# Kernel optimization log

Hardware: AMD Instinct MI355X
Metric: run time of the kernel (lower is better)

Reference implementation:

```python
import jax, jax.numpy as jnp
import numpy as np

DIM = 64
NUM_HEADS = 2
HEAD_DIM = DIM // NUM_HEADS


def setup_inputs() -> dict:
    key = jax.random.key(0)
    k1, k2, k3 = jax.random.split(key, 3)
    b, c, h, w = 8, DIM, 256, 256
    x = jax.random.normal(k1, (b, c, h, w), dtype=jnp.float32)
    # 1x1 conv weights, stored as [out_ch, in_ch] (kernel spatial dims are 1)
    qkv_w = jax.random.normal(k2, (3 * c, c), dtype=jnp.float32) * (1.0 / np.sqrt(c))
    proj_w = jax.random.normal(k3, (c, c), dtype=jnp.float32) * (1.0 / np.sqrt(c))
    return {"x": x, "qkv_w": qkv_w, "proj_w": proj_w}


def _phi(t):
    # elu(x) + 1 feature map (positive-valued kernel features)
    return jax.nn.elu(t) + 1.0


def reference(x, qkv_w, proj_w):
    b, c, h, w = x.shape
    n = h * w
    # 1x1 conv == per-pixel channel matmul
    qkv = jnp.einsum('oc,bchw->bohw', qkv_w, x)  # [b, 3c, h, w]
    q, k, v = jnp.split(qkv, 3, axis=1)

    def reshape(t):
        return t.reshape(b, NUM_HEADS, HEAD_DIM, n)  # bhcn

    q_phi = _phi(reshape(q))
    k_phi = _phi(reshape(k))
    v_h = reshape(v)
    # KV outer product over the sequence dim: tiny [b, h, c, d]
    KV = jnp.einsum('bhcn,bhdn->bhcd', k_phi, v_h)
    out_h = jnp.einsum('bhcn,bhcd->bhdn', q_phi, KV)  # [b, h, d, n]
    out = out_h.reshape(b, c, h, w)
    return jnp.einsum('oc,bchw->bohw', proj_w, out)
```

## Files before the change

### kernel.cpp

```cpp
#include <hip/hip_runtime.h>
#include <hip/hip_bf16.h>

#define BATCH 8
#define CH    64
#define NPIX  65536
#define NHEAD 2
#define HDIM  32
#define P1_BLOCKS 128

typedef __attribute__((ext_vector_type(8))) short bf16x8;
typedef __attribute__((ext_vector_type(4))) float f32x4;

#define MFMA(a, b, c) __builtin_amdgcn_mfma_f32_16x16x32_bf16(a, b, c, 0, 0, 0)

__device__ __forceinline__ unsigned rne_pk(float lo, float hi) {
    unsigned ua = __float_as_uint(lo); ua += 0x7fffu + ((ua >> 16) & 1u);
    unsigned ub = __float_as_uint(hi); ub += 0x7fffu + ((ub >> 16) & 1u);
    return (ua >> 16) | (ub & 0xffff0000u);
}

__device__ __forceinline__ bf16x8 pack8(const float* f) {
    int4 iv;
    iv.x = (int)rne_pk(f[0], f[1]);
    iv.y = (int)rne_pk(f[2], f[3]);
    iv.z = (int)rne_pk(f[4], f[5]);
    iv.w = (int)rne_pk(f[6], f[7]);
    return *reinterpret_cast<bf16x8*>(&iv);
}

__device__ __forceinline__ float phi_f(float t) {
    return t > 0.0f ? t + 1.0f : __expf(t);
}

__device__ __forceinline__ bf16x8 load_w_frag(const float* W, int r0, int k0, int lane) {
    const float* p = W + (size_t)(r0 + (lane & 15)) * 64 + k0 + ((lane >> 4) << 3);
    float f[8];
    #pragma unroll
    for (int e = 0; e < 8; e++) f[e] = p[e];
    return pack8(f);
}

__global__ __launch_bounds__(256) void la_pass1(
    const float* __restrict__ x, const float* __restrict__ qkv_w,
    float* __restrict__ partials, unsigned short* __restrict__ xt)
{
    __shared__ __align__(16) unsigned char smem[40960];

    const int tid  = threadIdx.x;
    const int lane = tid & 63;
    const int wv   = __builtin_amdgcn_readfirstlane(tid >> 6);
    const int b    = blockIdx.y;
    const int g    = lane >> 4;
    const int li   = lane & 15;

    unsigned short* kls = (unsigned short*)(smem + wv * 10240);
    unsigned short* vls = kls + 64 * 40;

    bf16x8 Wf[8][2];
    #pragma unroll
    for (int j = 0; j < 8; j++)
        #pragma unroll
        for (int ks = 0; ks < 2; ks++)
            Wf[j][ks] = load_w_frag(qkv_w, 64 + 16 * j, 32 * ks, lane);

    f32x4 kvacc[2][2][2];
    #pragma unroll
    for (int h = 0; h < 2; h++)
        #pragma unroll
        for (int mt = 0; mt < 2; mt++)
            #pragma unroll
            for (int nt = 0; nt < 2; nt++)
                kvacc[h][mt][nt] = (f32x4){0.f, 0.f, 0.f, 0.f};

    const float* xb = x + (size_t)b * CH * NPIX;
    unsigned short* xtb = xt + (size_t)b * NPIX * CH;

    for (int s = blockIdx.x * 4 + wv; s < 2048; s += P1_BLOCKS * 4) {
        const int px0 = s * 32;

        bf16x8 xa[2][2];
        #pragma unroll
        for (int mt = 0; mt < 2; mt++) {
            const float* xp = xb + px0 + 16 * mt + li;
            #pragma unroll
            for (int ks = 0; ks < 2; ks++) {
                float f[8];
                #pragma unroll
                for (int e = 0; e < 8; e++)
                    f[e] = xp[(size_t)(32 * ks + 8 * g + e) * NPIX];
                xa[mt][ks] = pack8(f);
            }
        }

        #pragma unroll
        for (int mt = 0; mt < 2; mt++)
            #pragma unroll
            for (int ks = 0; ks < 2; ks++)
                *reinterpret_cast<int4*>(xtb + (size_t)(px0 + 16 * mt + li) * CH + 32 * ks + 8 * g) =
                    *reinterpret_cast<const int4*>(&xa[mt][ks]);

        #pragma unroll
        for (int j = 0; j < 8; j++) {
            unsigned short* dst = (j < 4) ? kls : vls;
            const int crow = (j & 3) * 16 + li;
            #pragma unroll
            for (int mt = 0; mt < 2; mt++) {
                f32x4 acc = (f32x4){0.f, 0.f, 0.f, 0.f};
                acc = MFMA(xa[mt][0], Wf[j][0], acc);
                acc = MFMA(xa[mt][1], Wf[j][1], acc);
                float v0 = acc[0], v1 = acc[1], v2 = acc[2], v3 = acc[3];
                if (j < 4) { v0 = phi_f(v0); v1 = phi_f(v1); v2 = phi_f(v2); v3 = phi_f(v3); }
                *reinterpret_cast<uint2*>(dst + crow * 40 + 16 * mt + 4 * g) =
                    make_uint2(rne_pk(v0, v1), rne_pk(v2, v3));
            }
        }

        #pragma unroll
        for (int h = 0; h < 2; h++) {
            bf16x8 af[2], bv[2];
            #pragma unroll
            for (int mt = 0; mt < 2; mt++)
                af[mt] = *reinterpret_cast<const bf16x8*>(kls + (32 * h + 16 * mt + li) * 40 + 8 * g);
            #pragma unroll
            for (int nt = 0; nt < 2; nt++)
                bv[nt] = *reinterpret_cast<const bf16x8*>(vls + (32 * h + 16 * nt + li) * 40 + 8 * g);
            #pragma unroll
            for (int mt = 0; mt < 2; mt++)
                #pragma unroll
                for (int nt = 0; nt < 2; nt++)
                    kvacc[h][mt][nt] = MFMA(af[mt], bv[nt], kvacc[h][mt][nt]);
        }
    }

    __syncthreads();
    float* rbuf = (float*)smem;
    #pragma unroll
    for (int h = 0; h < 2; h++)
        #pragma unroll
        for (int mt = 0; mt < 2; mt++)
            #pragma unroll
            for (int nt = 0; nt < 2; nt++) {
                const int t = (h * 2 + mt) * 2 + nt;
                #pragma unroll
                for (int r = 0; r < 4; r++)
                    rbuf[wv * 2048 + t * 256 + (4 * g + r) * 16 + li] = kvacc[h][mt][nt][r];
            }
    __syncthreads();

    float* outp = partials + ((size_t)b * P1_BLOCKS + blockIdx.x) * 2048;
    #pragma unroll
    for (int i = 0; i < 8; i++) {
        const int idx = i * 256 + tid;
        const float sum = rbuf[idx] + rbuf[2048 + idx] + rbuf[4096 + idx] + rbuf[6144 + idx];
        const int t = idx >> 8, within = idx & 255;
        const int row = within >> 4, col = within & 15;
        const int h = t >> 2, mt = (t >> 1) & 1, nt = t & 1;
        outp[(h * 32 + 16 * mt + row) * 32 + 16 * nt + col] = sum;
    }
}

__global__ __launch_bounds__(256) void la_reduce(
    const float* __restrict__ partials, float* __restrict__ kv)
{
    const int b = blockIdx.x >> 3;
    const int e = (blockIdx.x & 7) * 256 + threadIdx.x;
    const float* p = partials + (size_t)b * P1_BLOCKS * 2048 + e;
    float s0 = 0.f, s1 = 0.f, s2 = 0.f, s3 = 0.f;
    #pragma unroll 8
    for (int j = 0; j < P1_BLOCKS; j += 4) {
        s0 += p[(size_t)j * 2048];
        s1 += p[(size_t)(j + 1) * 2048];
        s2 += p[(size_t)(j + 2) * 2048];
        s3 += p[(size_t)(j + 3) * 2048];
    }
    kv[(size_t)b * 2048 + e] = (s0 + s1) + (s2 + s3);
}

__global__ __launch_bounds__(256) void la_pass2(
    const unsigned short* __restrict__ xt, const float* __restrict__ qkv_w,
    const float* __restrict__ proj_w, const float* __restrict__ kv,
    float* __restrict__ y)
{
    __shared__ __align__(16) unsigned short sm2[4][2][16][72];

    const int tid  = threadIdx.x;
    const int lane = tid & 63;
    const int wv   = __builtin_amdgcn_readfirstlane(tid >> 6);
    const int b    = blockIdx.y;
    const int g    = lane >> 4;
    const int li   = lane & 15;

    unsigned short* qT = &sm2[wv][0][0][0];
    unsigned short* oT = &sm2[wv][1][0][0];

    bf16x8 Aq[4][2], Ap[4][2], Akv[2][2];
    #pragma unroll
    for (int mt = 0; mt < 4; mt++)
        #pragma unroll
        for (int ks = 0; ks < 2; ks++) {
            Aq[mt][ks] = load_w_frag(qkv_w, 16 * mt, 32 * ks, lane);
            Ap[mt][ks] = load_w_frag(proj_w, 16 * mt, 32 * ks, lane);
        }
    const float* kvb = kv + (size_t)b * NHEAD * HDIM * HDIM;
    #pragma unroll
    for (int h = 0; h < 2; h++)
        #pragma unroll
        for (int mtd = 0; mtd < 2; mtd++) {
            float f[8];
            #pragma unroll
            for (int e = 0; e < 8; e++)
                f[e] = kvb[h * 1024 + (8 * g + e) * 32 + 16 * mtd + li];
            Akv[h][mtd] = pack8(f);
        }

    const unsigned short* xtb = xt + (size_t)b * NPIX * CH;
    float*                yb  = y  + (size_t)b * CH * NPIX;

    for (int s = blockIdx.x * 4 + wv; s < 4096; s += 1024) {
        const int px0 = s * 16;

        bf16x8 bx[2];
        const unsigned short* xp = xtb + (size_t)(px0 + li) * CH + 8 * g;
        #pragma unroll
        for (int ks = 0; ks < 2; ks++)
            bx[ks] = *reinterpret_cast<const bf16x8*>(xp + 32 * ks);

        #pragma unroll
        for (int mt = 0; mt < 4; mt++) {
            f32x4 acc = (f32x4){0.f, 0.f, 0.f, 0.f};
            acc = MFMA(Aq[mt][0], bx[0], acc);
            acc = MFMA(Aq[mt][1], bx[1], acc);
            const float p0 = phi_f(acc[0]), p1 = phi_f(acc[1]);
            const float p2 = phi_f(acc[2]), p3 = phi_f(acc[3]);
            *reinterpret_cast<uint2*>(qT + li * 72 + 16 * mt + 4 * g) =
                make_uint2(rne_pk(p0, p1), rne_pk(p2, p3));
        }

        #pragma unroll
        for (int h = 0; h < 2; h++) {
            const bf16x8 bq = *reinterpret_cast<const bf16x8*>(qT + li * 72 + 32 * h + 8 * g);
            #pragma unroll
            for (int mtd = 0; mtd < 2; mtd++) {
                f32x4 acc = (f32x4){0.f, 0.f, 0.f, 0.f};
                acc = MFMA(Akv[h][mtd], bq, acc);
                *reinterpret_cast<uint2*>(oT + li * 72 + 32 * h + 16 * mtd + 4 * g) =
                    make_uint2(rne_pk(acc[0], acc[1]), rne_pk(acc[2], acc[3]));
            }
        }

        const bf16x8 bo0 = *reinterpret_cast<const bf16x8*>(oT + li * 72 + 8 * g);
        const bf16x8 bo1 = *reinterpret_cast<const bf16x8*>(oT + li * 72 + 32 + 8 * g);
        #pragma unroll
        for (int mt = 0; mt < 4; mt++) {
            f32x4 acc = (f32x4){0.f, 0.f, 0.f, 0.f};
            acc = MFMA(Ap[mt][0], bo0, acc);
            acc = MFMA(Ap[mt][1], bo1, acc);
            #pragma unroll
            for (int r = 0; r < 4; r++)
                yb[(size_t)(16 * mt + 4 * g + r) * NPIX + px0 + li] = acc[r];
        }
    }
}

extern "C" void kernel_launch(void* const* d_in, const int* in_sizes, int n_in,
                              void* d_out, int out_size, void* d_ws, size_t ws_size,
                              hipStream_t stream) {
    (void)in_sizes; (void)n_in; (void)out_size; (void)ws_size;
    const float* x      = (const float*)d_in[0];
    const float* qkv_w  = (const float*)d_in[1];
    const float* proj_w = (const float*)d_in[2];
    float* yout = (float*)d_out;

    unsigned short* xt      = (unsigned short*)d_ws;
    float*          partials = (float*)(xt + (size_t)BATCH * NPIX * CH);
    float*          kv       = partials + (size_t)BATCH * P1_BLOCKS * 2048;

    la_pass1 <<<dim3(P1_BLOCKS, BATCH), dim3(256), 0, stream>>>(x, qkv_w, partials, xt);
    la_reduce<<<dim3(64),               dim3(256), 0, stream>>>(partials, kv);
    la_pass2 <<<dim3(256, BATCH),       dim3(256), 0, stream>>>(xt, qkv_w, proj_w, kv, yout);
}
```

Before: 132.2 us.

## Stage x tiles through LDS with coalesced float4 loads in pass1

Pass1 now loads a 64x128 pixel tile of x cooperatively, with each lane reading float4 along the pixel dimension. It converts the tile to bf16 in shared memory, and the waves then gather MFMA fragments from LDS instead of issuing strided scalar global loads per channel. The k/v LDS row pitch is changed from 40 to 36 elements, with fragment reads split into two 8-byte loads. This adds block-wide barriers around each tile and uses more shared memory, which may reduce occupancy.

```diff
diff --git a/kernel.cpp b/kernel.cpp
--- a/kernel.cpp
+++ b/kernel.cpp
@@ -32,6 +32,13 @@
     return t > 0.0f ? t + 1.0f : __expf(t);
 }
 
+__device__ __forceinline__ bf16x8 lds_read8(const unsigned short* p) {
+    uint2 a = *reinterpret_cast<const uint2*>(p);
+    uint2 b = *reinterpret_cast<const uint2*>(p + 4);
+    int4 iv; iv.x = (int)a.x; iv.y = (int)a.y; iv.z = (int)b.x; iv.w = (int)b.y;
+    return *reinterpret_cast<bf16x8*>(&iv);
+}
+
 __device__ __forceinline__ bf16x8 load_w_frag(const float* W, int r0, int k0, int lane) {
     const float* p = W + (size_t)(r0 + (lane & 15)) * 64 + k0 + ((lane >> 4) << 3);
     float f[8];
@@ -44,7 +51,8 @@
     const float* __restrict__ x, const float* __restrict__ qkv_w,
     float* __restrict__ partials, unsigned short* __restrict__ xt)
 {
-    __shared__ __align__(16) unsigned char smem[40960];
+    __shared__ __align__(16) unsigned char smem[53248];
+    unsigned short* xls = (unsigned short*)smem;
 
     const int tid  = threadIdx.x;
     const int lane = tid & 63;
@@ -52,9 +60,11 @@
     const int b    = blockIdx.y;
     const int g    = lane >> 4;
     const int li   = lane & 15;
-
-    unsigned short* kls = (unsigned short*)(smem + wv * 10240);
-    unsigned short* vls = kls + 64 * 40;
+    const int l32  = lane & 31;
+    const int lhi  = lane >> 5;
+
+    unsigned short* kls = (unsigned short*)(smem + 16384 + wv * 9216);
+    unsigned short* vls = kls + 64 * 36;
 
     bf16x8 Wf[8][2];
     #pragma unroll
@@ -75,29 +85,47 @@
     const float* xb = x + (size_t)b * CH * NPIX;
     unsigned short* xtb = xt + (size_t)b * NPIX * CH;
 
-    for (int s = blockIdx.x * 4 + wv; s < 2048; s += P1_BLOCKS * 4) {
-        const int px0 = s * 32;
+    for (int it = 0; it < 4; it++) {
+        const int px0 = (blockIdx.x * 4 + it) * 128;
+
+        #pragma unroll
+        for (int j = 0; j < 8; j++) {
+            const int ch = wv * 16 + 2 * j + lhi;
+            const float4 f = *reinterpret_cast<const float4*>(
+                xb + (size_t)ch * NPIX + px0 + 4 * l32);
+            *reinterpret_cast<uint2*>(&xls[ch * 128 + 4 * l32]) =
+                make_uint2(rne_pk(f.x, f.y), rne_pk(f.z, f.w));
+        }
+        __syncthreads();
 
         bf16x8 xa[2][2];
         #pragma unroll
         for (int mt = 0; mt < 2; mt++) {
-            const float* xp = xb + px0 + 16 * mt + li;
+            const int px = 32 * wv + 16 * mt + li;
             #pragma unroll
             for (int ks = 0; ks < 2; ks++) {
-                float f[8];
-                #pragma unroll
-                for (int e = 0; e < 8; e++)
-                    f[e] = xp[(size_t)(32 * ks + 8 * g + e) * NPIX];
-                xa[mt][ks] = pack8(f);
+                const unsigned short* sp = &xls[(32 * ks + 8 * g) * 128 + px];
+                int4 iv;
+                {
+                    unsigned v0 = sp[0], v1 = sp[128], v2 = sp[256], v3 = sp[384];
+                    unsigned v4 = sp[512], v5 = sp[640], v6 = sp[768], v7 = sp[896];
+                    iv.x = (int)(v0 | (v1 << 16));
+                    iv.y = (int)(v2 | (v3 << 16));
+                    iv.z = (int)(v4 | (v5 << 16));
+                    iv.w = (int)(v6 | (v7 << 16));
+                }
+                xa[mt][ks] = *reinterpret_cast<bf16x8*>(&iv);
             }
         }
 
         #pragma unroll
-        for (int mt = 0; mt < 2; mt++)
+        for (int mt = 0; mt < 2; mt++) {
+            const int px = px0 + 32 * wv + 16 * mt + li;
             #pragma unroll
             for (int ks = 0; ks < 2; ks++)
-                *reinterpret_cast<int4*>(xtb + (size_t)(px0 + 16 * mt + li) * CH + 32 * ks + 8 * g) =
+                *reinterpret_cast<int4*>(xtb + (size_t)px * CH + 32 * ks + 8 * g) =
                     *reinterpret_cast<const int4*>(&xa[mt][ks]);
+        }
 
         #pragma unroll
         for (int j = 0; j < 8; j++) {
@@ -110,7 +138,7 @@
                 acc = MFMA(xa[mt][1], Wf[j][1], acc);
                 float v0 = acc[0], v1 = acc[1], v2 = acc[2], v3 = acc[3];
                 if (j < 4) { v0 = phi_f(v0); v1 = phi_f(v1); v2 = phi_f(v2); v3 = phi_f(v3); }
-                *reinterpret_cast<uint2*>(dst + crow * 40 + 16 * mt + 4 * g) =
+                *reinterpret_cast<uint2*>(dst + crow * 36 + 16 * mt + 4 * g) =
                     make_uint2(rne_pk(v0, v1), rne_pk(v2, v3));
             }
         }
@@ -120,19 +148,19 @@
             bf16x8 af[2], bv[2];
             #pragma unroll
             for (int mt = 0; mt < 2; mt++)
-                af[mt] = *reinterpret_cast<const bf16x8*>(kls + (32 * h + 16 * mt + li) * 40 + 8 * g);
+                af[mt] = lds_read8(kls + (32 * h + 16 * mt + li) * 36 + 8 * g);
             #pragma unroll
             for (int nt = 0; nt < 2; nt++)
-                bv[nt] = *reinterpret_cast<const bf16x8*>(vls + (32 * h + 16 * nt + li) * 40 + 8 * g);
+                bv[nt] = lds_read8(vls + (32 * h + 16 * nt + li) * 36 + 8 * g);
             #pragma unroll
             for (int mt = 0; mt < 2; mt++)
                 #pragma unroll
                 for (int nt = 0; nt < 2; nt++)
                     kvacc[h][mt][nt] = MFMA(af[mt], bv[nt], kvacc[h][mt][nt]);
         }
+        __syncthreads();
     }
 
-    __syncthreads();
     float* rbuf = (float*)smem;
     #pragma unroll
     for (int h = 0; h < 2; h++)
@@ -271,7 +299,7 @@
     const float* proj_w = (const float*)d_in[2];
     float* yout = (float*)d_out;
 
-    unsigned short* xt      = (unsigned short*)d_ws;
+    unsigned short* xt       = (unsigned short*)d_ws;
     float*          partials = (float*)(xt + (size_t)BATCH * NPIX * CH);
     float*          kv       = partials + (size_t)BATCH * P1_BLOCKS * 2048;
 
```

Measured after the change: 149.7 us. +13.2%, slower.

## Stage x tile in LDS with coalesced loads and keep K/V in registers

Applied to the files above, without the earlier changes.

Pass1 now loads a 64-channel by 256-pixel tile of x with float4 coalesced reads, converts it to bf16 in shared memory, and reads MFMA operands and the transposed xt output from there. The K·V outer product now takes the K/V fragments straight from registers via 16x16x16 MFMA instead of going through an LDS round trip. Pass2 writes the output with nontemporal stores. This trades strided scalar global loads for block-level syncs and LDS bank traffic in the transpose reads.

```diff
diff --git a/kernel.cpp b/kernel.cpp
--- a/kernel.cpp
+++ b/kernel.cpp
@@ -9,9 +9,18 @@
 #define P1_BLOCKS 128
 
 typedef __attribute__((ext_vector_type(8))) short bf16x8;
+typedef __attribute__((ext_vector_type(4))) short bf16x4;
 typedef __attribute__((ext_vector_type(4))) float f32x4;
 
-#define MFMA(a, b, c) __builtin_amdgcn_mfma_f32_16x16x32_bf16(a, b, c, 0, 0, 0)
+#define MFMA32(a, b, c) __builtin_amdgcn_mfma_f32_16x16x32_bf16(a, b, c, 0, 0, 0)
+
+#if __has_builtin(__builtin_amdgcn_mfma_f32_16x16x16_bf16)
+typedef __attribute__((ext_vector_type(4))) __bf16 bf16v4;
+#define MFMA16(a, b, c) __builtin_amdgcn_mfma_f32_16x16x16_bf16( \
+    __builtin_bit_cast(bf16v4, (a)), __builtin_bit_cast(bf16v4, (b)), (c), 0, 0, 0)
+#else
+#define MFMA16(a, b, c) __builtin_amdgcn_mfma_f32_16x16x16bf16_1k((a), (b), (c), 0, 0, 0)
+#endif
 
 __device__ __forceinline__ unsigned rne_pk(float lo, float hi) {
     unsigned ua = __float_as_uint(lo); ua += 0x7fffu + ((ua >> 16) & 1u);
@@ -44,7 +53,8 @@
     const float* __restrict__ x, const float* __restrict__ qkv_w,
     float* __restrict__ partials, unsigned short* __restrict__ xt)
 {
-    __shared__ __align__(16) unsigned char smem[40960];
+    __shared__ __align__(16) unsigned char smem[33024];
+    unsigned short* xls = (unsigned short*)smem;
 
     const int tid  = threadIdx.x;
     const int lane = tid & 63;
@@ -53,9 +63,6 @@
     const int g    = lane >> 4;
     const int li   = lane & 15;
 
-    unsigned short* kls = (unsigned short*)(smem + wv * 10240);
-    unsigned short* vls = kls + 64 * 40;
-
     bf16x8 Wf[8][2];
     #pragma unroll
     for (int j = 0; j < 8; j++)
@@ -67,83 +74,103 @@
     #pragma unroll
     for (int h = 0; h < 2; h++)
         #pragma unroll
-        for (int mt = 0; mt < 2; mt++)
+        for (int m2 = 0; m2 < 2; m2++)
             #pragma unroll
             for (int nt = 0; nt < 2; nt++)
-                kvacc[h][mt][nt] = (f32x4){0.f, 0.f, 0.f, 0.f};
+                kvacc[h][m2][nt] = (f32x4){0.f, 0.f, 0.f, 0.f};
 
     const float* xb = x + (size_t)b * CH * NPIX;
     unsigned short* xtb = xt + (size_t)b * NPIX * CH;
 
-    for (int s = blockIdx.x * 4 + wv; s < 2048; s += P1_BLOCKS * 4) {
-        const int px0 = s * 32;
-
-        bf16x8 xa[2][2];
-        #pragma unroll
-        for (int mt = 0; mt < 2; mt++) {
-            const float* xp = xb + px0 + 16 * mt + li;
+    for (int it = 0; it < 2; it++) {
+        const int px0 = (blockIdx.x * 2 + it) * 256;
+
+        #pragma unroll
+        for (int k4 = 0; k4 < 4; k4++) {
+            float4 f[4];
+            #pragma unroll
+            for (int k = 0; k < 4; k++)
+                f[k] = *reinterpret_cast<const float4*>(
+                    xb + (size_t)(wv + 4 * (4 * k4 + k)) * NPIX + px0 + 4 * lane);
+            #pragma unroll
+            for (int k = 0; k < 4; k++)
+                *reinterpret_cast<uint2*>(&xls[(wv + 4 * (4 * k4 + k)) * 258 + 4 * lane]) =
+                    make_uint2(rne_pk(f[k].x, f[k].y), rne_pk(f[k].z, f[k].w));
+        }
+        __syncthreads();
+
+        #pragma unroll
+        for (int mt = 0; mt < 4; mt++) {
+            const int pxl = 64 * wv + 16 * mt + li;
+
+            bf16x8 xa[2];
             #pragma unroll
             for (int ks = 0; ks < 2; ks++) {
-                float f[8];
+                unsigned v[8];
                 #pragma unroll
                 for (int e = 0; e < 8; e++)
-                    f[e] = xp[(size_t)(32 * ks + 8 * g + e) * NPIX];
-                xa[mt][ks] = pack8(f);
-            }
-        }
-
-        #pragma unroll
-        for (int mt = 0; mt < 2; mt++)
-            #pragma unroll
-            for (int ks = 0; ks < 2; ks++)
-                *reinterpret_cast<int4*>(xtb + (size_t)(px0 + 16 * mt + li) * CH + 32 * ks + 8 * g) =
-                    *reinterpret_cast<const int4*>(&xa[mt][ks]);
-
-        #pragma unroll
-        for (int j = 0; j < 8; j++) {
-            unsigned short* dst = (j < 4) ? kls : vls;
-            const int crow = (j & 3) * 16 + li;
-            #pragma unroll
-            for (int mt = 0; mt < 2; mt++) {
+                    v[e] = xls[(32 * ks + 8 * g + e) * 258 + pxl];
+                int4 iv;
+                iv.x = (int)(v[0] | (v[1] << 16));
+                iv.y = (int)(v[2] | (v[3] << 16));
+                iv.z = (int)(v[4] | (v[5] << 16));
+                iv.w = (int)(v[6] | (v[7] << 16));
+                xa[ks] = *reinterpret_cast<bf16x8*>(&iv);
+            }
+
+            bf16x4 kA[4], vB[4];
+            #pragma unroll
+            for (int j = 0; j < 8; j++) {
                 f32x4 acc = (f32x4){0.f, 0.f, 0.f, 0.f};
-                acc = MFMA(xa[mt][0], Wf[j][0], acc);
-                acc = MFMA(xa[mt][1], Wf[j][1], acc);
+                acc = MFMA32(xa[0], Wf[j][0], acc);
+                acc = MFMA32(xa[1], Wf[j][1], acc);
                 float v0 = acc[0], v1 = acc[1], v2 = acc[2], v3 = acc[3];
                 if (j < 4) { v0 = phi_f(v0); v1 = phi_f(v1); v2 = phi_f(v2); v3 = phi_f(v3); }
-                *reinterpret_cast<uint2*>(dst + crow * 40 + 16 * mt + 4 * g) =
-                    make_uint2(rne_pk(v0, v1), rne_pk(v2, v3));
-            }
-        }
-
-        #pragma unroll
-        for (int h = 0; h < 2; h++) {
-            bf16x8 af[2], bv[2];
-            #pragma unroll
-            for (int mt = 0; mt < 2; mt++)
-                af[mt] = *reinterpret_cast<const bf16x8*>(kls + (32 * h + 16 * mt + li) * 40 + 8 * g);
-            #pragma unroll
-            for (int nt = 0; nt < 2; nt++)
-                bv[nt] = *reinterpret_cast<const bf16x8*>(vls + (32 * h + 16 * nt + li) * 40 + 8 * g);
-            #pragma unroll
-            for (int mt = 0; mt < 2; mt++)
+                uint2 p = make_uint2(rne_pk(v0, v1), rne_pk(v2, v3));
+                bf16x4 r = __builtin_bit_cast(bf16x4, p);
+                if (j < 4) kA[j] = r; else vB[j - 4] = r;
+            }
+
+            #pragma unroll
+            for (int h = 0; h < 2; h++)
                 #pragma unroll
-                for (int nt = 0; nt < 2; nt++)
-                    kvacc[h][mt][nt] = MFMA(af[mt], bv[nt], kvacc[h][mt][nt]);
-        }
+                for (int m2 = 0; m2 < 2; m2++)
+                    #pragma unroll
+                    for (int nt = 0; nt < 2; nt++)
+                        kvacc[h][m2][nt] = MFMA16(kA[2 * h + m2], vB[2 * h + nt], kvacc[h][m2][nt]);
+        }
+
+        #pragma unroll
+        for (int seg = 0; seg < 4; seg++) {
+            const int pxl = 64 * seg + (tid >> 2);
+            const int c0  = (tid & 3) * 16;
+            unsigned d[8];
+            #pragma unroll
+            for (int i = 0; i < 8; i++) {
+                unsigned lo = xls[(c0 + 2 * i) * 258 + pxl];
+                unsigned hi = xls[(c0 + 2 * i + 1) * 258 + pxl];
+                d[i] = lo | (hi << 16);
+            }
+            unsigned short* dst = xtb + (size_t)(px0 + pxl) * CH + c0;
+            int4 lo4; lo4.x = (int)d[0]; lo4.y = (int)d[1]; lo4.z = (int)d[2]; lo4.w = (int)d[3];
+            int4 hi4; hi4.x = (int)d[4]; hi4.y = (int)d[5]; hi4.z = (int)d[6]; hi4.w = (int)d[7];
+            *reinterpret_cast<int4*>(dst)     = lo4;
+            *reinterpret_cast<int4*>(dst + 8) = hi4;
+        }
+        __syncthreads();
     }
 
-    __syncthreads();
     float* rbuf = (float*)smem;
     #pragma unroll
     for (int h = 0; h < 2; h++)
         #pragma unroll
-        for (int mt = 0; mt < 2; mt++)
+        for (int m2 = 0; m2 < 2; m2++)
             #pragma unroll
             for (int nt = 0; nt < 2; nt++) {
-                const int t = (h * 2 + mt) * 2 + nt;
+                const int t = (h * 2 + m2) * 2 + nt;
                 #pragma unroll
                 for (int r = 0; r < 4; r++)
-                    rbuf[wv * 2048 + t * 256 + (4 * g + r) * 16 + li] = kvacc[h][mt][nt][r];
+                    rbuf[wv * 2048 + t * 256 + (4 * g + r) * 16 + li] = kvacc[h][m2][nt][r];
             }
     __syncthreads();
 
@@ -154,8 +181,8 @@
         const float sum = rbuf[idx] + rbuf[2048 + idx] + rbuf[4096 + idx] + rbuf[6144 + idx];
         const int t = idx >> 8, within = idx & 255;
         const int row = within >> 4, col = within & 15;
-        const int h = t >> 2, mt = (t >> 1) & 1, nt = t & 1;
-        outp[(h * 32 + 16 * mt + row) * 32 + 16 * nt + col] = sum;
+        const int h = t >> 2, m2 = (t >> 1) & 1, nt = t & 1;
+        outp[(h * 32 + 16 * m2 + row) * 32 + 16 * nt + col] = sum;
     }
 }
 
@@ -221,15 +248,14 @@
 
         bf16x8 bx[2];
         const unsigned short* xp = xtb + (size_t)(px0 + li) * CH + 8 * g;
-        #pragma unroll
-        for (int ks = 0; ks < 2; ks++)
-            bx[ks] = *reinterpret_cast<const bf16x8*>(xp + 32 * ks);
+        bx[0] = *reinterpret_cast<const bf16x8*>(xp);
+        bx[1] = *reinterpret_cast<const bf16x8*>(xp + 32);
 
         #pragma unroll
         for (int mt = 0; mt < 4; mt++) {
             f32x4 acc = (f32x4){0.f, 0.f, 0.f, 0.f};
-            acc = MFMA(Aq[mt][0], bx[0], acc);
-            acc = MFMA(Aq[mt][1], bx[1], acc);
+            acc = MFMA32(Aq[mt][0], bx[0], acc);
+            acc = MFMA32(Aq[mt][1], bx[1], acc);
             const float p0 = phi_f(acc[0]), p1 = phi_f(acc[1]);
             const float p2 = phi_f(acc[2]), p3 = phi_f(acc[3]);
             *reinterpret_cast<uint2*>(qT + li * 72 + 16 * mt + 4 * g) =
@@ -242,7 +268,7 @@
             #pragma unroll
             for (int mtd = 0; mtd < 2; mtd++) {
                 f32x4 acc = (f32x4){0.f, 0.f, 0.f, 0.f};
-                acc = MFMA(Akv[h][mtd], bq, acc);
+                acc = MFMA32(Akv[h][mtd], bq, acc);
                 *reinterpret_cast<uint2*>(oT + li * 72 + 32 * h + 16 * mtd + 4 * g) =
                     make_uint2(rne_pk(acc[0], acc[1]), rne_pk(acc[2], acc[3]));
             }
@@ -253,11 +279,12 @@
         #pragma unroll
         for (int mt = 0; mt < 4; mt++) {
             f32x4 acc = (f32x4){0.f, 0.f, 0.f, 0.f};
-            acc = MFMA(Ap[mt][0], bo0, acc);
-            acc = MFMA(Ap[mt][1], bo1, acc);
+            acc = MFMA32(Ap[mt][0], bo0, acc);
+            acc = MFMA32(Ap[mt][1], bo1, acc);
             #pragma unroll
             for (int r = 0; r < 4; r++)
-                yb[(size_t)(16 * mt + 4 * g + r) * NPIX + px0 + li] = acc[r];
+                __builtin_nontemporal_store(acc[r],
+                    &yb[(size_t)(16 * mt + 4 * g + r) * NPIX + px0 + li]);
         }
     }
 }
@@ -271,11 +298,11 @@
     const float* proj_w = (const float*)d_in[2];
     float* yout = (float*)d_out;
 
-    unsigned short* xt      = (unsigned short*)d_ws;
-    float*          partials = (float*)(xt + (size_t)BATCH * NPIX * CH);
+    unsigned short* xtw      = (unsigned short*)d_ws;
+    float*          partials = (float*)(xtw + (size_t)BATCH * NPIX * CH);
     float*          kv       = partials + (size_t)BATCH * P1_BLOCKS * 2048;
 
-    la_pass1 <<<dim3(P1_BLOCKS, BATCH), dim3(256), 0, stream>>>(x, qkv_w, partials, xt);
+    la_pass1 <<<dim3(P1_BLOCKS, BATCH), dim3(256), 0, stream>>>(x, qkv_w, partials, xtw);
     la_reduce<<<dim3(64),               dim3(256), 0, stream>>>(partials, kv);
-    la_pass2 <<<dim3(256, BATCH),       dim3(256), 0, stream>>>(xt, qkv_w, proj_w, kv, yout);
-}
+    la_pass2 <<<dim3(256, BATCH),       dim3(256), 0, stream>>>(xtw, qkv_w, proj_w, kv, yout);
+}
```

New measurement: 125.5 us. 1.05x faster.
